# Kernel optimization log

Hardware: AMD Instinct MI355X
Metric: run time of the kernel (lower is better)

Reference implementation:

```python
import jax, jax.numpy as jnp
import numpy as np

N_NODES = 100_000
N_EDGES = 1_600_000
F_NODE = 16
F_EDGE = 8
HID = 128
N_GRAPHS = 2048


def setup_inputs() -> dict:
    key = jax.random.key(0)
    ks = jax.random.split(key, 20)
    inp = {
        "node_attr": jax.random.normal(ks[0], (N_NODES, F_NODE), dtype=jnp.float32),
        "edge_attr": jax.random.normal(ks[1], (N_EDGES, F_EDGE), dtype=jnp.float32),
        "edge_index": jax.random.randint(ks[2], (2, N_EDGES), 0, N_NODES),
        "adj_index": jax.random.randint(ks[3], (2, N_EDGES), 0, N_NODES),
        "adj_value": jax.random.uniform(ks[4], (N_EDGES,), dtype=jnp.float32) * 0.1,
        "batch": jnp.sort(jax.random.randint(ks[5], (N_NODES,), 0, N_GRAPHS)),
    }
    def glorot(k, shape):
        fan_in, fan_out = shape[0], shape[1]
        std = jnp.sqrt(2.0 / (fan_in + fan_out)).astype(jnp.float32)
        return jax.random.normal(k, shape, dtype=jnp.float32) * std
    # attr embedder params
    inp["W_node"] = glorot(ks[6], (F_NODE, HID))
    inp["W_edge"] = glorot(ks[7], (F_EDGE, HID))
    inp["b_embed"] = jnp.zeros((HID,), dtype=jnp.float32)
    # 3 GCN layers
    inp["W1"] = glorot(ks[8], (HID, HID)); inp["b1"] = jnp.zeros((HID,), jnp.float32)
    inp["W2"] = glorot(ks[9], (HID, HID)); inp["b2"] = jnp.zeros((HID,), jnp.float32)
    inp["W3"] = glorot(ks[10], (HID, HID)); inp["b3"] = jnp.zeros((HID,), jnp.float32)
    # predictor MLP
    inp["Wp1"] = glorot(ks[11], (HID, HID)); inp["bp1"] = jnp.full((HID,), 0.01, jnp.float32)
    inp["Wp2"] = glorot(ks[12], (HID, 1));   inp["bp2"] = jnp.full((1,), 0.01, jnp.float32)
    return inp


def _forward(node_attr, edge_attr, adj_value,
             W_node, W_edge, b_embed, W1, b1, W2, b2, W3, b3,
             Wp1, bp1, Wp2, bp2, edge_index, adj_index, batch):
    # --- attr embedder: mix node feats with edge feats scattered to dst nodes ---
    he = edge_attr @ W_edge                                   # [E, H]
    agg = jax.ops.segment_sum(he, edge_index[1], num_segments=N_NODES)
    h = jax.nn.relu(node_attr @ W_node + agg + b_embed)       # [N, H]

    # --- GCN stack: h <- relu(tilde_A @ (h W) + b) via sparse COO SpMM ---
    src, dst = adj_index[0], adj_index[1]
    def gcn(h, W, b):
        hw = h @ W + b                                        # [N, H]
        msg = adj_value[:, None] * hw[dst]                    # [E, H] gather
        return jax.nn.relu(jax.ops.segment_sum(msg, src, num_segments=N_NODES))
    h = gcn(h, W1, b1)
    h = gcn(h, W2, b2)
    h = gcn(h, W3, b3)

    # --- global_add_pool over graphs ---
    fp = jax.ops.segment_sum(h, batch, num_segments=N_GRAPHS)  # [G, H]

    # --- predictor MLP ---
    z = jax.nn.relu(fp @ Wp1 + bp1)
    return z @ Wp2 + bp2                                       # [G, 1]


def reference(node_attr, edge_attr, edge_index, adj_index, adj_value, batch,
              W_node, W_edge, b_embed, W1, b1, W2, b2, W3, b3,
              Wp1, bp1, Wp2, bp2):
    return _forward(node_attr, edge_attr, adj_value,
                    W_node, W_edge, b_embed, W1, b1, W2, b2, W3, b3,
                    Wp1, bp1, Wp2, bp2, edge_index, adj_index, batch)
```

## Files before the change

kernel.cpp:

```cpp
#include <hip/hip_runtime.h>

#define H 128
#define FN 16
#define FE 8
#define NBUK_MAX 1600

__global__ __launch_bounds__(256) void k_hist2(
    const int* __restrict__ k1, const int* __restrict__ k2,
    int* __restrict__ bcnt1, int* __restrict__ bcnt2, int E, int nbuk) {
  __shared__ int h1[NBUK_MAX], h2[NBUK_MAX];
  for (int i = threadIdx.x; i < nbuk; i += 256) { h1[i] = 0; h2[i] = 0; }
  __syncthreads();
  for (int e = blockIdx.x * 256 + threadIdx.x; e < E; e += gridDim.x * 256) {
    atomicAdd(&h1[k1[e] >> 6], 1);
    atomicAdd(&h2[k2[e] >> 6], 1);
  }
  __syncthreads();
  for (int i = threadIdx.x; i < nbuk; i += 256) {
    if (h1[i]) atomicAdd(&bcnt1[i], h1[i]);
    if (h2[i]) atomicAdd(&bcnt2[i], h2[i]);
  }
}

__global__ __launch_bounds__(1024) void k_scan(
    const int* __restrict__ cnt1, int* __restrict__ st1, int* __restrict__ gc1,
    const int* __restrict__ cnt2, int* __restrict__ st2, int* __restrict__ gc2,
    int nbuk) {
  __shared__ int s[1024];
  int tid = threadIdx.x;
  for (int pass = 0; pass < 2; pass++) {
    const int* cnt = pass ? cnt2 : cnt1;
    int* st = pass ? st2 : st1;
    int* gc = pass ? gc2 : gc1;
    int run = 0;
    for (int half = 0; half * 1024 < nbuk; half++) {
      int i = half * 1024 + tid;
      int v = (i < nbuk) ? cnt[i] : 0;
      s[tid] = v; __syncthreads();
      for (int off = 1; off < 1024; off <<= 1) {
        int t = (tid >= off) ? s[tid - off] : 0;
        __syncthreads();
        s[tid] += t;
        __syncthreads();
      }
      int excl = run + s[tid] - v;
      if (i < nbuk) { st[i] = excl; gc[i] = excl; }
      run += s[1023];
      __syncthreads();
    }
    if (tid == 0) st[nbuk] = run;
    __syncthreads();
  }
}

template <int PACKED>
__global__ __launch_bounds__(256) void k_p1_scatter(
    const int* __restrict__ key, const int* __restrict__ dsts,
    const float* __restrict__ vals, int* __restrict__ gcur,
    int* __restrict__ pkey, int2* __restrict__ bpay, int E, int nbuk) {
  __shared__ int hc[NBUK_MAX];
  int tid = threadIdx.x;
  int c0 = blockIdx.x * 8192;
  int c1 = min(c0 + 8192, E);
  for (int i = tid; i < nbuk; i += 256) hc[i] = 0;
  __syncthreads();
  for (int e = c0 + tid; e < c1; e += 256)
    atomicAdd(&hc[key[e] >> 6], 1);
  __syncthreads();
  for (int i = tid; i < nbuk; i += 256) {
    int c = hc[i];
    if (c) hc[i] = atomicAdd(&gcur[i], c);
  }
  __syncthreads();
  for (int e = c0 + tid; e < c1; e += 256) {
    int k = key[e];
    int pos = atomicAdd(&hc[k >> 6], 1);
    if (PACKED) {
      pkey[pos] = (e << 6) | (k & 63);
    } else {
      bpay[pos] = make_int2(dsts[e] | ((k & 63) << 20), __float_as_int(vals[e]));
    }
  }
}

__global__ __launch_bounds__(256) void k_embed_agg(
    const int* __restrict__ pkey, const float* __restrict__ edge_attr,
    const int* __restrict__ bstart, float* __restrict__ agg8, int N) {
  __shared__ float lds[FE][64];
  int b = blockIdx.x, tid = threadIdx.x;
  for (int i = tid; i < FE * 64; i += 256) ((float*)lds)[i] = 0.f;
  __syncthreads();
  int s = bstart[b], t = bstart[b + 1];
  int i = s + tid;
  for (; i + 256 < t; i += 512) {
    int pk0 = pkey[i], pk1 = pkey[i + 256];
    const float4* e0 = (const float4*)(edge_attr + (size_t)(pk0 >> 6) * FE);
    const float4* e1 = (const float4*)(edge_attr + (size_t)(pk1 >> 6) * FE);
    float4 a0 = e0[0], b0 = e0[1], a1 = e1[0], b1 = e1[1];
    int s0 = pk0 & 63, s1 = pk1 & 63;
    atomicAdd(&lds[0][s0], a0.x);  atomicAdd(&lds[1][s0], a0.y);
    atomicAdd(&lds[2][s0], a0.z);  atomicAdd(&lds[3][s0], a0.w);
    atomicAdd(&lds[4][s0], b0.x);  atomicAdd(&lds[5][s0], b0.y);
    atomicAdd(&lds[6][s0], b0.z);  atomicAdd(&lds[7][s0], b0.w);
    atomicAdd(&lds[0][s1], a1.x);  atomicAdd(&lds[1][s1], a1.y);
    atomicAdd(&lds[2][s1], a1.z);  atomicAdd(&lds[3][s1], a1.w);
    atomicAdd(&lds[4][s1], b1.x);  atomicAdd(&lds[5][s1], b1.y);
    atomicAdd(&lds[6][s1], b1.z);  atomicAdd(&lds[7][s1], b1.w);
  }
  for (; i < t; i += 256) {
    int pk = pkey[i];
    int e = pk >> 6, slot = pk & 63;
    const float4* ea = (const float4*)(edge_attr + (size_t)e * FE);
    float4 a = ea[0], b4 = ea[1];
    atomicAdd(&lds[0][slot], a.x);  atomicAdd(&lds[1][slot], a.y);
    atomicAdd(&lds[2][slot], a.z);  atomicAdd(&lds[3][slot], a.w);
    atomicAdd(&lds[4][slot], b4.x); atomicAdd(&lds[5][slot], b4.y);
    atomicAdd(&lds[6][slot], b4.z); atomicAdd(&lds[7][slot], b4.w);
  }
  __syncthreads();
  int node0 = b * 64;
  for (int j = tid; j < 64 * FE; j += 256) {
    int n = node0 + (j >> 3);
    if (n < N) agg8[(size_t)n * FE + (j & 7)] = lds[j & 7][j >> 3];
  }
}

__global__ __launch_bounds__(256) void k_p2(
    const int2* __restrict__ bpay, const int* __restrict__ bstart,
    int* __restrict__ offs, int2* __restrict__ payF, int N, int E) {
  __shared__ int cnt[64], scn[64], cur[64];
  int b = blockIdx.x, tid = threadIdx.x;
  int s = bstart[b], t = bstart[b + 1];
  if (tid < 64) cnt[tid] = 0;
  __syncthreads();
  for (int i = s + tid; i < t; i += 256) atomicAdd(&cnt[(bpay[i].x >> 20) & 63], 1);
  __syncthreads();
  if (tid < 64) scn[tid] = cnt[tid];
  __syncthreads();
  for (int off = 1; off < 64; off <<= 1) {
    int v = 0;
    if (tid < 64 && tid >= off) v = scn[tid - off];
    __syncthreads();
    if (tid < 64 && tid >= off) scn[tid] += v;
    __syncthreads();
  }
  if (tid < 64) {
    int excl = s + scn[tid] - cnt[tid];
    cur[tid] = excl;
    int node = b * 64 + tid;
    if (node < N) offs[node] = excl;
  }
  if (b == 0 && tid == 0) offs[N] = E;
  __syncthreads();
  for (int i = s + tid; i < t; i += 256) {
    int2 p = bpay[i];
    int slot = (p.x >> 20) & 63;
    int pos = atomicAdd(&cur[slot], 1);
    payF[pos] = make_int2(p.x & 0xFFFFF, p.y);
  }
}

__global__ __launch_bounds__(256) void k_embed_h(
    const float* __restrict__ node_attr, const float* __restrict__ Wn,
    const float* __restrict__ We8, const float* __restrict__ b,
    const float* __restrict__ agg8, float* __restrict__ h, int N) {
  __shared__ float Ws[FN * H];
  __shared__ float Es[FE * H];
  __shared__ float na[2][FN];
  __shared__ float a8[2][FE];
  for (int i = threadIdx.x; i < FN * H; i += 256) Ws[i] = Wn[i];
  for (int i = threadIdx.x; i < FE * H; i += 256) Es[i] = We8[i];
  int lane = threadIdx.x & 127;
  int sub  = threadIdx.x >> 7;
  for (int n0 = blockIdx.x * 2; n0 < N; n0 += gridDim.x * 2) {
    int n = n0 + sub;
    __syncthreads();
    if (n < N) {
      if (lane < FN) na[sub][lane] = node_attr[(size_t)n * FN + lane];
      else if (lane < FN + FE) a8[sub][lane - FN] = agg8[(size_t)n * FE + (lane - FN)];
    }
    __syncthreads();
    if (n < N) {
      float acc = b[lane];
#pragma unroll
      for (int k = 0; k < FN; k++) acc += na[sub][k] * Ws[k * H + lane];
#pragma unroll
      for (int k = 0; k < FE; k++) acc += a8[sub][k] * Es[k * H + lane];
      h[(size_t)n * H + lane] = fmaxf(acc, 0.f);
    }
  }
}

template <int RELU_OUT>
__global__ __launch_bounds__(256) void k_gemm(
    const float* __restrict__ in, const float* __restrict__ W,
    const float* __restrict__ bias, float* __restrict__ out, int N) {
  __shared__ float4 hs4[64 * 32];
  int tid = threadIdx.x;
  int c  = tid & 31;
  int rg = tid >> 5;
  int rowBase = blockIdx.x * 64;
  const float4* in4 = (const float4*)in;
  const float4* W4  = (const float4*)W;

#pragma unroll
  for (int j = 0; j < 8; j++) {
    int q = tid + 256 * j;
    int r = rowBase + (q >> 5);
    int rr = (r < N) ? r : (N - 1);
    hs4[q] = in4[(size_t)rr * 32 + (q & 31)];
  }
  __syncthreads();

  float4 acc[8];
#pragma unroll
  for (int i = 0; i < 8; i++) acc[i] = make_float4(0.f, 0.f, 0.f, 0.f);

#pragma unroll 2
  for (int k = 0; k < 32; k++) {
    float4 w0 = W4[(k * 4 + 0) * 32 + c];
    float4 w1 = W4[(k * 4 + 1) * 32 + c];
    float4 w2 = W4[(k * 4 + 2) * 32 + c];
    float4 w3 = W4[(k * 4 + 3) * 32 + c];
#pragma unroll
    for (int i = 0; i < 8; i++) {
      float4 hv = hs4[(rg + 8 * i) * 32 + k];
      acc[i].x += hv.x * w0.x + hv.y * w1.x + hv.z * w2.x + hv.w * w3.x;
      acc[i].y += hv.x * w0.y + hv.y * w1.y + hv.z * w2.y + hv.w * w3.y;
      acc[i].z += hv.x * w0.z + hv.y * w1.z + hv.z * w2.z + hv.w * w3.z;
      acc[i].w += hv.x * w0.w + hv.y * w1.w + hv.z * w2.w + hv.w * w3.w;
    }
  }

  float4 bv = ((const float4*)bias)[c];
#pragma unroll
  for (int i = 0; i < 8; i++) {
    int row = rowBase + rg + 8 * i;
    if (row < N) {
      float4 o = make_float4(acc[i].x + bv.x, acc[i].y + bv.y,
                             acc[i].z + bv.z, acc[i].w + bv.w);
      if (RELU_OUT) {
        o.x = fmaxf(o.x, 0.f); o.y = fmaxf(o.y, 0.f);
        o.z = fmaxf(o.z, 0.f); o.w = fmaxf(o.w, 0.f);
      }
      ((float4*)out)[(size_t)row * 32 + c] = o;
    }
  }
}

__global__ __launch_bounds__(256) void k_gcn_gather(
    const float* __restrict__ hw, const int* __restrict__ offs,
    const int2* __restrict__ pay, float* __restrict__ out, int N) {
  int n = blockIdx.x * 8 + (threadIdx.x >> 5);
  if (n >= N) return;
  int c = threadIdx.x & 31;
  int s = offs[n], t = offs[n + 1];
  const float4* hw4 = (const float4*)hw;
  float4 a0 = make_float4(0.f, 0.f, 0.f, 0.f);
  float4 a1 = make_float4(0.f, 0.f, 0.f, 0.f);
  float4 a2 = make_float4(0.f, 0.f, 0.f, 0.f);
  float4 a3 = make_float4(0.f, 0.f, 0.f, 0.f);
  int i = s;
  int t4 = s + ((t - s) & ~3);
  for (; i < t4; i += 4) {
    int2 p0 = pay[i], p1 = pay[i + 1], p2 = pay[i + 2], p3 = pay[i + 3];
    float4 h0 = hw4[(size_t)p0.x * 32 + c];
    float4 h1 = hw4[(size_t)p1.x * 32 + c];
    float4 h2 = hw4[(size_t)p2.x * 32 + c];
    float4 h3 = hw4[(size_t)p3.x * 32 + c];
    float v0 = __int_as_float(p0.y), v1 = __int_as_float(p1.y);
    float v2 = __int_as_float(p2.y), v3 = __int_as_float(p3.y);
    a0.x += v0 * h0.x; a0.y += v0 * h0.y; a0.z += v0 * h0.z; a0.w += v0 * h0.w;
    a1.x += v1 * h1.x; a1.y += v1 * h1.y; a1.z += v1 * h1.z; a1.w += v1 * h1.w;
    a2.x += v2 * h2.x; a2.y += v2 * h2.y; a2.z += v2 * h2.z; a2.w += v2 * h2.w;
    a3.x += v3 * h3.x; a3.y += v3 * h3.y; a3.z += v3 * h3.z; a3.w += v3 * h3.w;
  }
  for (; i < t; i++) {
    int2 p = pay[i];
    float v = __int_as_float(p.y);
    float4 hv = hw4[(size_t)p.x * 32 + c];
    a0.x += v * hv.x; a0.y += v * hv.y; a0.z += v * hv.z; a0.w += v * hv.w;
  }
  float4 o;
  o.x = fmaxf(a0.x + a1.x + a2.x + a3.x, 0.f);
  o.y = fmaxf(a0.y + a1.y + a2.y + a3.y, 0.f);
  o.z = fmaxf(a0.z + a1.z + a2.z + a3.z, 0.f);
  o.w = fmaxf(a0.w + a1.w + a2.w + a3.w, 0.f);
  ((float4*)(out + (size_t)n * H))[c] = o;
}

__global__ __launch_bounds__(256) void k_gbounds(
    const int* __restrict__ batch, int* __restrict__ gstart, int N, int G) {
  int n = blockIdx.x * 256 + threadIdx.x;
  if (n > N) return;
  if (n == 0) {
    for (int g = 0; g <= batch[0]; g++) gstart[g] = 0;
  } else if (n == N) {
    for (int g = batch[N - 1] + 1; g <= G; g++) gstart[g] = N;
  } else {
    int b0 = batch[n - 1], b1 = batch[n];
    for (int g = b0 + 1; g <= b1; g++) gstart[g] = n;
  }
}

__global__ __launch_bounds__(128) void k_pool_seg(
    const float* __restrict__ h, const int* __restrict__ gstart,
    float* __restrict__ fp, int G) {
  int g = blockIdx.x;
  int j = threadIdx.x;
  int s = gstart[g], t = gstart[g + 1];
  float acc = 0.f;
  for (int n = s; n < t; n++) acc += h[(size_t)n * H + j];
  fp[(size_t)g * H + j] = acc;
}

__global__ __launch_bounds__(256) void k_pred2(
    const float* __restrict__ z, const float* __restrict__ Wp2,
    const float* __restrict__ bp2, float* __restrict__ out, int G) {
  int g = blockIdx.x * 4 + (threadIdx.x >> 6);
  if (g >= G) return;
  int l = threadIdx.x & 63;
  float2 zv = ((const float2*)z)[(size_t)g * 64 + l];
  float2 wv = ((const float2*)Wp2)[l];
  float v = zv.x * wv.x + zv.y * wv.y;
#pragma unroll
  for (int off = 32; off > 0; off >>= 1) v += __shfl_down(v, off, 64);
  if (l == 0) out[g] = v + bp2[0];
}

extern "C" void kernel_launch(void* const* d_in, const int* in_sizes, int n_in,
                              void* d_out, int out_size, void* d_ws, size_t ws_size,
                              hipStream_t stream) {
  const float* node_attr  = (const float*)d_in[0];
  const float* edge_attr  = (const float*)d_in[1];
  const int*   edge_index = (const int*)d_in[2];
  const int*   adj_index  = (const int*)d_in[3];
  const float* adj_value  = (const float*)d_in[4];
  const int*   batch      = (const int*)d_in[5];
  const float* W_node  = (const float*)d_in[6];
  const float* W_edge  = (const float*)d_in[7];
  const float* b_embed = (const float*)d_in[8];
  const float* W1 = (const float*)d_in[9];
  const float* b1 = (const float*)d_in[10];
  const float* W2 = (const float*)d_in[11];
  const float* b2 = (const float*)d_in[12];
  const float* W3 = (const float*)d_in[13];
  const float* b3 = (const float*)d_in[14];
  const float* Wp1 = (const float*)d_in[15];
  const float* bp1 = (const float*)d_in[16];
  const float* Wp2 = (const float*)d_in[17];
  const float* bp2 = (const float*)d_in[18];
  float* out = (float*)d_out;

  const int E = in_sizes[4];
  const int N = in_sizes[5];
  const int G = out_size;
  const int nbuk = (N + 63) >> 6;
  const int p1b = (E + 8191) / 8192;

  float* A     = (float*)d_ws;
  float* B     = A + (size_t)N * H;
  int2*  payF  = (int2*)(B + (size_t)N * H);
  float* fpool = (float*)(payF + E);
  int*   bcnt1 = (int*)(fpool + (size_t)G * H);
  int*   bcnt2 = bcnt1 + nbuk;
  int*   bst1  = bcnt2 + nbuk;
  int*   gcur1 = bst1 + nbuk + 1;
  int*   bst2  = gcur1 + nbuk;
  int*   gcur2 = bst2 + nbuk + 1;
  int*   offs2 = gcur2 + nbuk;
  int*   gstart= offs2 + N + 1;
  float* agg8  = A;
  int*   pkey  = (int*)B;
  int2*  bpay2 = (int2*)(((int*)B) + E);
  float* zbuf  = A;

  hipMemsetAsync(bcnt1, 0, (size_t)2 * nbuk * sizeof(int), stream);
  k_hist2<<<512, 256, 0, stream>>>(edge_index + E, adj_index, bcnt1, bcnt2, E, nbuk);
  k_scan<<<1, 1024, 0, stream>>>(bcnt1, bst1, gcur1, bcnt2, bst2, gcur2, nbuk);

  k_p1_scatter<1><<<p1b, 256, 0, stream>>>(edge_index + E, nullptr, nullptr,
                                           gcur1, pkey, nullptr, E, nbuk);
  k_p1_scatter<0><<<p1b, 256, 0, stream>>>(adj_index, adj_index + E, adj_value,
                                           gcur2, nullptr, bpay2, E, nbuk);

  k_embed_agg<<<nbuk, 256, 0, stream>>>(pkey, edge_attr, bst1, agg8, N);
  k_p2<<<nbuk, 256, 0, stream>>>(bpay2, bst2, offs2, payF, N, E);

  k_embed_h<<<4096, 256, 0, stream>>>(node_attr, W_node, W_edge, b_embed, agg8, B, N);

  k_gbounds<<<(N + 256) / 256, 256, 0, stream>>>(batch, gstart, N, G);

  int gemm_blocks = (N + 63) / 64;
  int agb = (N + 7) / 8;
  k_gemm<0><<<gemm_blocks, 256, 0, stream>>>(B, W1, b1, A, N);
  k_gcn_gather<<<agb, 256, 0, stream>>>(A, offs2, payF, B, N);
  k_gemm<0><<<gemm_blocks, 256, 0, stream>>>(B, W2, b2, A, N);
  k_gcn_gather<<<agb, 256, 0, stream>>>(A, offs2, payF, B, N);
  k_gemm<0><<<gemm_blocks, 256, 0, stream>>>(B, W3, b3, A, N);
  k_gcn_gather<<<agb, 256, 0, stream>>>(A, offs2, payF, B, N);

  k_pool_seg<<<G, 128, 0, stream>>>(B, gstart, fpool, G);
  k_gemm<1><<<G / 64, 256, 0, stream>>>(fpool, Wp1, bp1, zbuf, G);
  k_pred2<<<(G + 3) / 4, 256, 0, stream>>>(zbuf, Wp2, bp2, out, G);
}
```

Before: 968.0 us.

## Fuse GCN gather and GEMM by reordering aggregation before weight multiply

Each GCN layer now aggregates neighbour features first (A·h) into shared memory and then multiplies by W in the same kernel. The bias is folded in as the per-node sum of adjacency values, which is computed during the CSR build. This removes three separate kernel launches and the N×H round trip through global memory between the GEMM and the gather. The cost is that each block serially gathers 8 rows per wavefront group before the GEMM, so there is less parallelism across nodes and latency is harder to hide during the gather.

```diff
diff --git a/kernel.cpp b/kernel.cpp
--- a/kernel.cpp
+++ b/kernel.cpp
@@ -127,11 +127,13 @@
 
 __global__ __launch_bounds__(256) void k_p2(
     const int2* __restrict__ bpay, const int* __restrict__ bstart,
-    int* __restrict__ offs, int2* __restrict__ payF, int N, int E) {
+    int* __restrict__ offs, int2* __restrict__ payF, float* __restrict__ rs,
+    int N, int E) {
   __shared__ int cnt[64], scn[64], cur[64];
+  __shared__ float vsum[64];
   int b = blockIdx.x, tid = threadIdx.x;
   int s = bstart[b], t = bstart[b + 1];
-  if (tid < 64) cnt[tid] = 0;
+  if (tid < 64) { cnt[tid] = 0; vsum[tid] = 0.f; }
   __syncthreads();
   for (int i = s + tid; i < t; i += 256) atomicAdd(&cnt[(bpay[i].x >> 20) & 63], 1);
   __syncthreads();
@@ -157,6 +159,12 @@
     int slot = (p.x >> 20) & 63;
     int pos = atomicAdd(&cur[slot], 1);
     payF[pos] = make_int2(p.x & 0xFFFFF, p.y);
+    atomicAdd(&vsum[slot], __int_as_float(p.y));
+  }
+  __syncthreads();
+  if (tid < 64) {
+    int node = b * 64 + tid;
+    if (node < N) rs[node] = vsum[tid];
   }
 }
 
@@ -191,6 +199,92 @@
   }
 }
 
+__global__ __launch_bounds__(256) void k_fused(
+    const float* __restrict__ h, const int* __restrict__ offs,
+    const int2* __restrict__ pay, const float* __restrict__ W,
+    const float* __restrict__ bias, const float* __restrict__ rs,
+    float* __restrict__ out, int N) {
+  __shared__ float4 hs4[64 * 32];
+  int tid = threadIdx.x;
+  int c  = tid & 31;
+  int rg = tid >> 5;
+  int base = blockIdx.x * 64;
+  const float4* h4 = (const float4*)h;
+
+  for (int r = 0; r < 8; r++) {
+    int row = rg * 8 + r;
+    int n = base + row;
+    float4 a0 = make_float4(0.f, 0.f, 0.f, 0.f);
+    float4 a1 = make_float4(0.f, 0.f, 0.f, 0.f);
+    float4 a2 = make_float4(0.f, 0.f, 0.f, 0.f);
+    float4 a3 = make_float4(0.f, 0.f, 0.f, 0.f);
+    if (n < N) {
+      int s = offs[n], t = offs[n + 1];
+      int i = s, t4 = s + ((t - s) & ~3);
+      for (; i < t4; i += 4) {
+        int2 p0 = pay[i], p1 = pay[i + 1], p2 = pay[i + 2], p3 = pay[i + 3];
+        float4 h0 = h4[(size_t)p0.x * 32 + c];
+        float4 h1 = h4[(size_t)p1.x * 32 + c];
+        float4 h2 = h4[(size_t)p2.x * 32 + c];
+        float4 h3 = h4[(size_t)p3.x * 32 + c];
+        float v0 = __int_as_float(p0.y), v1 = __int_as_float(p1.y);
+        float v2 = __int_as_float(p2.y), v3 = __int_as_float(p3.y);
+        a0.x += v0 * h0.x; a0.y += v0 * h0.y; a0.z += v0 * h0.z; a0.w += v0 * h0.w;
+        a1.x += v1 * h1.x; a1.y += v1 * h1.y; a1.z += v1 * h1.z; a1.w += v1 * h1.w;
+        a2.x += v2 * h2.x; a2.y += v2 * h2.y; a2.z += v2 * h2.z; a2.w += v2 * h2.w;
+        a3.x += v3 * h3.x; a3.y += v3 * h3.y; a3.z += v3 * h3.z; a3.w += v3 * h3.w;
+      }
+      for (; i < t; i++) {
+        int2 p = pay[i];
+        float v = __int_as_float(p.y);
+        float4 hv = h4[(size_t)p.x * 32 + c];
+        a0.x += v * hv.x; a0.y += v * hv.y; a0.z += v * hv.z; a0.w += v * hv.w;
+      }
+    }
+    hs4[row * 32 + c] = make_float4(a0.x + a1.x + a2.x + a3.x,
+                                    a0.y + a1.y + a2.y + a3.y,
+                                    a0.z + a1.z + a2.z + a3.z,
+                                    a0.w + a1.w + a2.w + a3.w);
+  }
+  __syncthreads();
+
+  const float4* W4 = (const float4*)W;
+  float4 acc[8];
+#pragma unroll
+  for (int i = 0; i < 8; i++) acc[i] = make_float4(0.f, 0.f, 0.f, 0.f);
+#pragma unroll 2
+  for (int k = 0; k < 32; k++) {
+    float4 w0 = W4[(k * 4 + 0) * 32 + c];
+    float4 w1 = W4[(k * 4 + 1) * 32 + c];
+    float4 w2 = W4[(k * 4 + 2) * 32 + c];
+    float4 w3 = W4[(k * 4 + 3) * 32 + c];
+#pragma unroll
+    for (int i = 0; i < 8; i++) {
+      float4 hv = hs4[(rg + 8 * i) * 32 + k];
+      acc[i].x += hv.x * w0.x + hv.y * w1.x + hv.z * w2.x + hv.w * w3.x;
+      acc[i].y += hv.x * w0.y + hv.y * w1.y + hv.z * w2.y + hv.w * w3.y;
+      acc[i].z += hv.x * w0.z + hv.y * w1.z + hv.z * w2.z + hv.w * w3.z;
+      acc[i].w += hv.x * w0.w + hv.y * w1.w + hv.z * w2.w + hv.w * w3.w;
+    }
+  }
+
+  float4 bv = ((const float4*)bias)[c];
+#pragma unroll
+  for (int i = 0; i < 8; i++) {
+    int row = rg + 8 * i;
+    int n = base + row;
+    if (n < N) {
+      float rsv = rs[n];
+      float4 o;
+      o.x = fmaxf(acc[i].x + rsv * bv.x, 0.f);
+      o.y = fmaxf(acc[i].y + rsv * bv.y, 0.f);
+      o.z = fmaxf(acc[i].z + rsv * bv.z, 0.f);
+      o.w = fmaxf(acc[i].w + rsv * bv.w, 0.f);
+      ((float4*)out)[(size_t)n * 32 + c] = o;
+    }
+  }
+}
+
 template <int RELU_OUT>
 __global__ __launch_bounds__(256) void k_gemm(
     const float* __restrict__ in, const float* __restrict__ W,
@@ -202,7 +296,6 @@
   int rowBase = blockIdx.x * 64;
   const float4* in4 = (const float4*)in;
   const float4* W4  = (const float4*)W;
-
 #pragma unroll
   for (int j = 0; j < 8; j++) {
     int q = tid + 256 * j;
@@ -211,11 +304,9 @@
     hs4[q] = in4[(size_t)rr * 32 + (q & 31)];
   }
   __syncthreads();
-
   float4 acc[8];
 #pragma unroll
   for (int i = 0; i < 8; i++) acc[i] = make_float4(0.f, 0.f, 0.f, 0.f);
-
 #pragma unroll 2
   for (int k = 0; k < 32; k++) {
     float4 w0 = W4[(k * 4 + 0) * 32 + c];
@@ -231,7 +322,6 @@
       acc[i].w += hv.x * w0.w + hv.y * w1.w + hv.z * w2.w + hv.w * w3.w;
     }
   }
-
   float4 bv = ((const float4*)bias)[c];
 #pragma unroll
   for (int i = 0; i < 8; i++) {
@@ -246,47 +336,6 @@
       ((float4*)out)[(size_t)row * 32 + c] = o;
     }
   }
-}
-
-__global__ __launch_bounds__(256) void k_gcn_gather(
-    const float* __restrict__ hw, const int* __restrict__ offs,
-    const int2* __restrict__ pay, float* __restrict__ out, int N) {
-  int n = blockIdx.x * 8 + (threadIdx.x >> 5);
-  if (n >= N) return;
-  int c = threadIdx.x & 31;
-  int s = offs[n], t = offs[n + 1];
-  const float4* hw4 = (const float4*)hw;
-  float4 a0 = make_float4(0.f, 0.f, 0.f, 0.f);
-  float4 a1 = make_float4(0.f, 0.f, 0.f, 0.f);
-  float4 a2 = make_float4(0.f, 0.f, 0.f, 0.f);
-  float4 a3 = make_float4(0.f, 0.f, 0.f, 0.f);
-  int i = s;
-  int t4 = s + ((t - s) & ~3);
-  for (; i < t4; i += 4) {
-    int2 p0 = pay[i], p1 = pay[i + 1], p2 = pay[i + 2], p3 = pay[i + 3];
-    float4 h0 = hw4[(size_t)p0.x * 32 + c];
-    float4 h1 = hw4[(size_t)p1.x * 32 + c];
-    float4 h2 = hw4[(size_t)p2.x * 32 + c];
-    float4 h3 = hw4[(size_t)p3.x * 32 + c];
-    float v0 = __int_as_float(p0.y), v1 = __int_as_float(p1.y);
-    float v2 = __int_as_float(p2.y), v3 = __int_as_float(p3.y);
-    a0.x += v0 * h0.x; a0.y += v0 * h0.y; a0.z += v0 * h0.z; a0.w += v0 * h0.w;
-    a1.x += v1 * h1.x; a1.y += v1 * h1.y; a1.z += v1 * h1.z; a1.w += v1 * h1.w;
-    a2.x += v2 * h2.x; a2.y += v2 * h2.y; a2.z += v2 * h2.z; a2.w += v2 * h2.w;
-    a3.x += v3 * h3.x; a3.y += v3 * h3.y; a3.z += v3 * h3.z; a3.w += v3 * h3.w;
-  }
-  for (; i < t; i++) {
-    int2 p = pay[i];
-    float v = __int_as_float(p.y);
-    float4 hv = hw4[(size_t)p.x * 32 + c];
-    a0.x += v * hv.x; a0.y += v * hv.y; a0.z += v * hv.z; a0.w += v * hv.w;
-  }
-  float4 o;
-  o.x = fmaxf(a0.x + a1.x + a2.x + a3.x, 0.f);
-  o.y = fmaxf(a0.y + a1.y + a2.y + a3.y, 0.f);
-  o.z = fmaxf(a0.z + a1.z + a2.z + a3.z, 0.f);
-  o.w = fmaxf(a0.w + a1.w + a2.w + a3.w, 0.f);
-  ((float4*)(out + (size_t)n * H))[c] = o;
 }
 
 __global__ __launch_bounds__(256) void k_gbounds(
@@ -370,10 +419,11 @@
   int*   gcur2 = bst2 + nbuk + 1;
   int*   offs2 = gcur2 + nbuk;
   int*   gstart= offs2 + N + 1;
+  float* rs    = (float*)(gstart + G + 1);
   float* agg8  = A;
   int*   pkey  = (int*)B;
   int2*  bpay2 = (int2*)(((int*)B) + E);
-  float* zbuf  = A;
+  float* zbuf  = B;
 
   hipMemsetAsync(bcnt1, 0, (size_t)2 * nbuk * sizeof(int), stream);
   k_hist2<<<512, 256, 0, stream>>>(edge_index + E, adj_index, bcnt1, bcnt2, E, nbuk);
@@ -385,22 +435,18 @@
                                            gcur2, nullptr, bpay2, E, nbuk);
 
   k_embed_agg<<<nbuk, 256, 0, stream>>>(pkey, edge_attr, bst1, agg8, N);
-  k_p2<<<nbuk, 256, 0, stream>>>(bpay2, bst2, offs2, payF, N, E);
+  k_p2<<<nbuk, 256, 0, stream>>>(bpay2, bst2, offs2, payF, rs, N, E);
 
   k_embed_h<<<4096, 256, 0, stream>>>(node_attr, W_node, W_edge, b_embed, agg8, B, N);
 
   k_gbounds<<<(N + 256) / 256, 256, 0, stream>>>(batch, gstart, N, G);
 
-  int gemm_blocks = (N + 63) / 64;
-  int agb = (N + 7) / 8;
-  k_gemm<0><<<gemm_blocks, 256, 0, stream>>>(B, W1, b1, A, N);
-  k_gcn_gather<<<agb, 256, 0, stream>>>(A, offs2, payF, B, N);
-  k_gemm<0><<<gemm_blocks, 256, 0, stream>>>(B, W2, b2, A, N);
-  k_gcn_gather<<<agb, 256, 0, stream>>>(A, offs2, payF, B, N);
-  k_gemm<0><<<gemm_blocks, 256, 0, stream>>>(B, W3, b3, A, N);
-  k_gcn_gather<<<agb, 256, 0, stream>>>(A, offs2, payF, B, N);
-
-  k_pool_seg<<<G, 128, 0, stream>>>(B, gstart, fpool, G);
-  k_gemm<1><<<G / 64, 256, 0, stream>>>(fpool, Wp1, bp1, zbuf, G);
+  int lb = (N + 63) / 64;
+  k_fused<<<lb, 256, 0, stream>>>(B, offs2, payF, W1, b1, rs, A, N);
+  k_fused<<<lb, 256, 0, stream>>>(A, offs2, payF, W2, b2, rs, B, N);
+  k_fused<<<lb, 256, 0, stream>>>(B, offs2, payF, W3, b3, rs, A, N);
+
+  k_pool_seg<<<G, 128, 0, stream>>>(A, gstart, fpool, G);
+  k_gemm<1><<<(G + 63) / 64, 256, 0, stream>>>(fpool, Wp1, bp1, zbuf, G);
   k_pred2<<<(G + 3) / 4, 256, 0, stream>>>(zbuf, Wp2, bp2, out, G);
 }
```

Measured after the change: 947.3 us. 1.02x faster.
